# Kernel optimization log

Measured on AMD Instinct MI355X. Metric: run time of the kernel, lower is better.

The kernel has to match this reference:

```python
import jax, jax.numpy as jnp
import numpy as np

B, S, D, H, F = 8, 1024, 1024, 16, 4096
DH = D // H
LN_EPS = 1e-3  # keras LayerNormalization default


def layer_norm(x, g, b, eps=LN_EPS):
    m = jnp.mean(x, axis=-1, keepdims=True)
    v = jnp.mean(jnp.square(x - m), axis=-1, keepdims=True)
    return (x - m) * jax.lax.rsqrt(v + eps) * g + b


def setup_inputs() -> dict:
    key = jax.random.key(0)
    ks = jax.random.split(key, 16)
    s = 0.02
    return {
        "x": jax.random.normal(ks[0], (B, S, D), dtype=jnp.float32),
        "key_padding_mask": jax.random.randint(ks[1], (B, S), 0, 2) > 0,
        "wq": jax.random.normal(ks[2], (D, D), dtype=jnp.float32) * s,
        "wk": jax.random.normal(ks[3], (D, D), dtype=jnp.float32) * s,
        "wv": jax.random.normal(ks[4], (D, D), dtype=jnp.float32) * s,
        "wo": jax.random.normal(ks[5], (D, D), dtype=jnp.float32) * s,
        "gamma": jnp.ones((H,), dtype=jnp.float32),
        "ln_g": jnp.ones((3, D), dtype=jnp.float32),   # pre_attn, post_attn, pre_fc
        "ln_b": jnp.zeros((3, D), dtype=jnp.float32),
        "ln_fc_g": jnp.ones((F,), dtype=jnp.float32),  # post_fc_norm over fc_dim
        "ln_fc_b": jnp.zeros((F,), dtype=jnp.float32),
        "w1": jax.random.normal(ks[6], (D, F), dtype=jnp.float32) * s,
        "b1": jnp.zeros((F,), dtype=jnp.float32),
        "w2": jax.random.normal(ks[7], (F, D), dtype=jnp.float32) * s,
        "b2": jnp.zeros((D,), dtype=jnp.float32),
        "lam": jnp.ones((D,), dtype=jnp.float32),
    }


def reference(x, key_padding_mask, wq, wk, wv, wo, gamma, ln_g, ln_b,
              ln_fc_g, ln_fc_b, w1, b1, w2, b2, lam):
    # ---- attention sub-block (self-attention path, x_clt=None) ----
    residual = x
    h = layer_norm(x, ln_g[0], ln_b[0])                       # pre_attn_norm
    q = (h @ wq).reshape(B, S, H, DH)
    k = (h @ wk).reshape(B, S, H, DH)
    v = (h @ wv).reshape(B, S, H, DH)
    scores = jnp.einsum('bqhd,bkhd->bhqk', q, k) / jnp.sqrt(jnp.float32(DH))
    # key_padding_mask: True = masked key
    scores = jnp.where(key_padding_mask[:, None, None, :], -1e9, scores)
    v = jnp.where(key_padding_mask[:, :, None, None], 0.0, v)
    attn = jax.nn.softmax(scores, axis=-1)
    ws = jnp.einsum('bhqk,bkhd->bqhd', attn, v)
    ws = ws * gamma[None, None, :, None]                      # per-head scale
    out = ws.reshape(B, S, D) @ wo
    out = layer_norm(out, ln_g[1], ln_b[1])                   # post_attn_norm
    x = out + residual
    # ---- FFN sub-block ----
    residual = x
    h = layer_norm(x, ln_g[2], ln_b[2])                       # pre_fc_norm
    h = jax.nn.gelu(h @ w1 + b1, approximate=False)
    h = layer_norm(h, ln_fc_g, ln_fc_b)                       # post_fc_norm (fc_dim)
    h = h @ w2 + b2
    return h + residual * lam
```

## Files before the change

kernel.cpp:

```cpp
#include <hip/hip_runtime.h>
#include <math.h>

typedef _Float16 h_t;
typedef _Float16 h8 __attribute__((ext_vector_type(8)));
typedef _Float16 h4 __attribute__((ext_vector_type(4)));
typedef float    f4 __attribute__((ext_vector_type(4)));
typedef unsigned int u32;

#define SEQ   1024
#define DIM   1024
#define FDIM  4096
#define NB    8
#define NH    16
#define DHD   64
#define NROWS 8192

__device__ __forceinline__ void glds16(const void* g, void* l)
{
    __builtin_amdgcn_global_load_lds((const __attribute__((address_space(1))) u32*)g,
                                     (__attribute__((address_space(3))) u32*)l, 16, 0, 0);
}

__global__ __launch_bounds__(256)
void canon_mask_k(const void* __restrict__ raw, int* __restrict__ outm, int n)
{
    const unsigned int*  w  = (const unsigned int*)raw;
    const unsigned char* cb = (const unsigned char*)raw;
    __shared__ int flag;
    if (threadIdx.x == 0) flag = 0;
    __syncthreads();
    int bad = 0;
    for (int i = threadIdx.x; i < 1024; i += 256)
        if (w[i] > 1u) bad = 1;
    if (bad) flag = 1;
    __syncthreads();
    const bool is_i32 = (flag == 0);
    const int idx = blockIdx.x * 256 + threadIdx.x;
    if (idx < n) outm[idx] = is_i32 ? (w[idx] != 0u) : (cb[idx] != 0);
}

__global__ __launch_bounds__(256)
void wconv_k(const float* __restrict__ W, h_t* __restrict__ Wt, int K, int N)
{
    __shared__ float T[32][33];
    const int t  = threadIdx.x;
    const int k0 = blockIdx.y * 32, n0 = blockIdx.x * 32;
    const int r = t >> 3, c4 = (t & 7) * 4;
    const float4 v = *(const float4*)(W + (size_t)(k0 + r) * N + n0 + c4);
    T[r][c4 + 0] = v.x; T[r][c4 + 1] = v.y; T[r][c4 + 2] = v.z; T[r][c4 + 3] = v.w;
    __syncthreads();
    h4 o = { (h_t)T[c4 + 0][r], (h_t)T[c4 + 1][r], (h_t)T[c4 + 2][r], (h_t)T[c4 + 3][r] };
    *(h4*)(Wt + (size_t)(n0 + r) * K + k0 + c4) = o;
}

__device__ __forceinline__ void block_reduce2(float& s, float& ss)
{
    #pragma unroll
    for (int off = 32; off > 0; off >>= 1) {
        s  += __shfl_down(s,  off, 64);
        ss += __shfl_down(ss, off, 64);
    }
    __shared__ float sh[8];
    const int wid  = threadIdx.x >> 6;
    const int lane = threadIdx.x & 63;
    if (lane == 0) { sh[wid] = s; sh[4 + wid] = ss; }
    __syncthreads();
    s  = sh[0] + sh[1] + sh[2] + sh[3];
    ss = sh[4] + sh[5] + sh[6] + sh[7];
}

template<typename TI, bool RES>
__global__ __launch_bounds__(256)
void ln1024_k(const TI* __restrict__ in, const float* __restrict__ gw,
              const float* __restrict__ bw, const float* __restrict__ res,
              h_t* __restrict__ out)
{
    const size_t base = (size_t)blockIdx.x * 1024;
    const int c = threadIdx.x * 4;
    float v[4];
    if constexpr (sizeof(TI) == 2) {
        h4 x = *(const h4*)(in + base + c);
        v[0] = (float)x[0]; v[1] = (float)x[1]; v[2] = (float)x[2]; v[3] = (float)x[3];
    } else {
        float4 x = *(const float4*)((const float*)in + base + c);
        v[0] = x.x; v[1] = x.y; v[2] = x.z; v[3] = x.w;
    }
    float s = v[0] + v[1] + v[2] + v[3];
    float ss = v[0]*v[0] + v[1]*v[1] + v[2]*v[2] + v[3]*v[3];
    block_reduce2(s, ss);
    const float mean = s * (1.f / 1024.f);
    const float rstd = rsqrtf(ss * (1.f / 1024.f) - mean * mean + 1e-3f);
    const float4 g4 = *(const float4*)(gw + c);
    const float4 b4 = *(const float4*)(bw + c);
    float o[4];
    o[0] = (v[0]-mean)*rstd*g4.x + b4.x; o[1] = (v[1]-mean)*rstd*g4.y + b4.y;
    o[2] = (v[2]-mean)*rstd*g4.z + b4.z; o[3] = (v[3]-mean)*rstd*g4.w + b4.w;
    if constexpr (RES) {
        const float4 r4 = *(const float4*)(res + base + c);
        o[0] += r4.x; o[1] += r4.y; o[2] += r4.z; o[3] += r4.w;
    }
    h4 oh = {(h_t)o[0], (h_t)o[1], (h_t)o[2], (h_t)o[3]};
    *(h4*)(out + base + c) = oh;
}

__global__ __launch_bounds__(256)
void ln4096_k(h_t* __restrict__ buf, const float* __restrict__ gw,
              const float* __restrict__ bw)
{
    const size_t base = (size_t)blockIdx.x * 4096;
    const int t = threadIdx.x;
    float v[16];
    #pragma unroll
    for (int i = 0; i < 2; ++i) {
        h8 x = *(const h8*)(buf + base + (i * 256 + t) * 8);
        #pragma unroll
        for (int j = 0; j < 8; ++j) v[i * 8 + j] = (float)x[j];
    }
    float s = 0.f, ss = 0.f;
    #pragma unroll
    for (int i = 0; i < 16; ++i) { s += v[i]; ss += v[i] * v[i]; }
    block_reduce2(s, ss);
    const float mean = s * (1.f / 4096.f);
    const float rstd = rsqrtf(ss * (1.f / 4096.f) - mean * mean + 1e-3f);
    #pragma unroll
    for (int i = 0; i < 2; ++i) {
        const int c = (i * 256 + t) * 8;
        h8 o;
        #pragma unroll
        for (int j = 0; j < 8; ++j)
            o[j] = (h_t)((v[i*8+j] - mean) * rstd * gw[c + j] + bw[c + j]);
        *(h8*)(buf + base + c) = o;
    }
}

#define GEPI_QK   0
#define GEPI_VT   1
#define GEPI_H16  2
#define GEPI_GELU 3
#define GEPI_FC2  4

__device__ __forceinline__ float gelu_exact(float x)
{
    return 0.5f * x * (1.f + erff(x * 0.70710678118654752440f));
}

template<int EPI>
__global__ __launch_bounds__(256, 2)
void hgemm_k(const h_t* __restrict__ A, const h_t* __restrict__ Wt,
             const float* __restrict__ bias, void* __restrict__ outv,
             int M, int K, int N,
             const int* __restrict__ mask, const h_t* __restrict__ resid,
             const float* __restrict__ lam)
{
    __shared__ h_t As[128 * 32];
    __shared__ h_t Bs[128 * 32];
    const int t = threadIdx.x;
    const int wv = t >> 6, lane = t & 63;
    const int m0 = blockIdx.y * 128, n0 = blockIdx.x * 128;
    const int wr = (wv >> 1) * 64, wc = (wv & 1) * 64;
    const int lr = lane & 15, g = lane >> 4;
    const int srow_base = (lane >> 2);
    const int sslot = (lane & 3) * 16;

    f4 acc[4][4] = {};

    for (int k0 = 0; k0 < K; k0 += 32) {
        __syncthreads();
        #pragma unroll
        for (int i = 0; i < 2; ++i) {
            const int rA = (wv * 2 + i) * 16 + srow_base;
            const int swz = ((rA >> 1) & 3) << 4;
            glds16((const char*)A  + (((size_t)(m0 + rA) * K + k0) << 1) + (sslot ^ swz),
                   (char*)As + (wv * 2 + i) * 1024);
            glds16((const char*)Wt + (((size_t)(n0 + rA) * K + k0) << 1) + (sslot ^ swz),
                   (char*)Bs + (wv * 2 + i) * 1024);
        }
        __syncthreads();
        h8 af[4], bf[4];
        #pragma unroll
        for (int mt = 0; mt < 4; ++mt) {
            const int r = wr + mt * 16 + lr;
            af[mt] = *(const h8*)((const char*)As + r * 64 + ((g * 16) ^ (((r >> 1) & 3) << 4)));
        }
        #pragma unroll
        for (int nt = 0; nt < 4; ++nt) {
            const int r = wc + nt * 16 + lr;
            bf[nt] = *(const h8*)((const char*)Bs + r * 64 + ((g * 16) ^ (((r >> 1) & 3) << 4)));
        }
        #pragma unroll
        for (int mt = 0; mt < 4; ++mt)
            #pragma unroll
            for (int nt = 0; nt < 4; ++nt)
                acc[mt][nt] = __builtin_amdgcn_mfma_f32_16x16x32_f16(af[mt], bf[nt], acc[mt][nt], 0, 0, 0);
    }

    #pragma unroll
    for (int mt = 0; mt < 4; ++mt) {
        #pragma unroll
        for (int nt = 0; nt < 4; ++nt) {
            #pragma unroll
            for (int e = 0; e < 4; ++e) {
                const int row = m0 + wr + mt * 16 + g * 4 + e;
                const int col = n0 + wc + nt * 16 + lr;
                float val = acc[mt][nt][e];
                if constexpr (EPI == GEPI_QK) {
                    const int b = row >> 10, s = row & 1023, hh = col >> 6, dd = col & 63;
                    ((h_t*)outv)[(((size_t)(b * NH + hh)) * SEQ + s) * DHD + dd] = (h_t)val;
                } else if constexpr (EPI == GEPI_VT) {
                    if (mask[row]) val = 0.f;
                    const int b = row >> 10, s = row & 1023, hh = col >> 6, dd = col & 63;
                    ((h_t*)outv)[(((size_t)(b * NH + hh)) * DHD + dd) * SEQ + s] = (h_t)val;
                } else if constexpr (EPI == GEPI_H16) {
                    ((h_t*)outv)[(size_t)row * N + col] = (h_t)val;
                } else if constexpr (EPI == GEPI_GELU) {
                    ((h_t*)outv)[(size_t)row * N + col] = (h_t)gelu_exact(val + bias[col]);
                } else {
                    val += bias[col] + (float)resid[(size_t)row * N + col] * lam[col];
                    ((float*)outv)[(size_t)row * N + col] = val;
                }
            }
        }
    }
}

__global__ __launch_bounds__(256)
void attn_k(const h_t* __restrict__ Q, const h_t* __restrict__ K,
            const h_t* __restrict__ Vt, const int* __restrict__ mask,
            const float* __restrict__ gamma, h_t* __restrict__ out)
{
    __shared__ h_t Kt[64 * 64];
    __shared__ h_t Vs[64 * 64];
    __shared__ h_t Pl[4 * 16 * 64];
    __shared__ float madd[64];
    const int t = threadIdx.x, wv = t >> 6, lane = t & 63;
    const int lr = lane & 15, g = lane >> 4;
    const int b = blockIdx.z, h = blockIdx.y, q0 = blockIdx.x * 64;
    const size_t qkbase = ((size_t)(b * NH + h)) * SEQ * DHD;
    const size_t vbase  = ((size_t)(b * NH + h)) * DHD * SEQ;

    h8 qf[2];
    {
        const h_t* qp = Q + qkbase + (size_t)(q0 + wv * 16 + lr) * DHD;
        const h_t sc = (h_t)0.125f;
        qf[0] = *(const h8*)(qp + 8 * g) * sc;
        qf[1] = *(const h8*)(qp + 32 + 8 * g) * sc;
    }

    f4 o[4] = {};
    float mrun = -3.0e38f, lrun = 0.f;
    h_t* pw = Pl + wv * 1024;

    for (int kt = 0; kt < SEQ / 64; ++kt) {
        const int kv0 = kt * 64;
        __syncthreads();
        #pragma unroll
        for (int i = 0; i < 2; ++i) {
            const int r = (wv * 2 + i) * 8 + (lane >> 3);
            const int slot = (lane & 7) * 16;
            glds16((const char*)K  + ((qkbase + (size_t)(kv0 + r) * DHD) << 1) + (slot ^ ((r & 7) << 4)),
                   (char*)Kt + (wv * 2 + i) * 1024);
            glds16((const char*)Vt + ((vbase + (size_t)r * SEQ + kv0) << 1) + (slot ^ ((r & 7) << 4)),
                   (char*)Vs + (wv * 2 + i) * 1024);
        }
        if (t < 64) madd[t] = mask[b * SEQ + kv0 + t] ? -1e9f : 0.f;
        __syncthreads();

        f4 s[4] = {};
        #pragma unroll
        for (int tt = 0; tt < 4; ++tt) {
            #pragma unroll
            for (int c = 0; c < 2; ++c) {
                const int r = tt * 16 + lr;
                h8 kf = *(const h8*)((const char*)Kt + r * 128 + ((c * 64 + g * 16) ^ ((r & 7) << 4)));
                s[tt] = __builtin_amdgcn_mfma_f32_16x16x32_f16(kf, qf[c], s[tt], 0, 0, 0);
            }
        }
        float mt_ = -3.0e38f;
        #pragma unroll
        for (int tt = 0; tt < 4; ++tt) {
            f4 ma = *(const f4*)(&madd[tt * 16 + g * 4]);
            s[tt] += ma;
            mt_ = fmaxf(mt_, fmaxf(fmaxf(s[tt][0], s[tt][1]), fmaxf(s[tt][2], s[tt][3])));
        }
        mt_ = fmaxf(mt_, __shfl_xor(mt_, 16, 64));
        mt_ = fmaxf(mt_, __shfl_xor(mt_, 32, 64));
        const float mnew = fmaxf(mrun, mt_);
        const float scl  = __expf(mrun - mnew);
        mrun = mnew;
        float ps = 0.f;
        #pragma unroll
        for (int tt = 0; tt < 4; ++tt) {
            const float p0 = __expf(s[tt][0] - mnew), p1 = __expf(s[tt][1] - mnew);
            const float p2 = __expf(s[tt][2] - mnew), p3 = __expf(s[tt][3] - mnew);
            ps += p0 + p1 + p2 + p3;
            h4 pq = {(h_t)p0, (h_t)p1, (h_t)p2, (h_t)p3};
            *(h4*)((char*)pw + lr * 128 + ((tt * 32 + g * 8) ^ ((lr & 7) << 4))) = pq;
        }
        ps += __shfl_xor(ps, 16, 64);
        ps += __shfl_xor(ps, 32, 64);
        lrun = lrun * scl + ps;

        #pragma unroll
        for (int e = 0; e < 4; ++e) {
            const float sce = __shfl(scl, g * 4 + e, 64);
            #pragma unroll
            for (int dt = 0; dt < 4; ++dt) o[dt][e] *= sce;
        }
        #pragma unroll
        for (int c = 0; c < 2; ++c) {
            h8 pa = *(const h8*)((const char*)pw + lr * 128 + ((c * 64 + g * 16) ^ ((lr & 7) << 4)));
            #pragma unroll
            for (int dt = 0; dt < 4; ++dt) {
                const int r = dt * 16 + lr;
                h8 vf = *(const h8*)((const char*)Vs + r * 128 + ((c * 64 + g * 16) ^ ((r & 7) << 4)));
                o[dt] = __builtin_amdgcn_mfma_f32_16x16x32_f16(pa, vf, o[dt], 0, 0, 0);
            }
        }
    }
    const float gm = gamma[h];
    #pragma unroll
    for (int e = 0; e < 4; ++e) {
        const float inv = gm / __shfl(lrun, g * 4 + e, 64);
        const int row = q0 + wv * 16 + g * 4 + e;
        #pragma unroll
        for (int dt = 0; dt < 4; ++dt)
            out[(size_t)(b * SEQ + row) * DIM + h * DHD + dt * 16 + lr] = (h_t)(o[dt][e] * inv);
    }
}

extern "C" void kernel_launch(void* const* d_in, const int* in_sizes, int n_in,
                              void* d_out, int out_size, void* d_ws, size_t ws_size,
                              hipStream_t stream)
{
    const float* x       = (const float*)d_in[0];
    const void*  kpm     = d_in[1];
    const float* wq      = (const float*)d_in[2];
    const float* wk      = (const float*)d_in[3];
    const float* wv      = (const float*)d_in[4];
    const float* wo      = (const float*)d_in[5];
    const float* gamma   = (const float*)d_in[6];
    const float* ln_g    = (const float*)d_in[7];
    const float* ln_b    = (const float*)d_in[8];
    const float* ln_fc_g = (const float*)d_in[9];
    const float* ln_fc_b = (const float*)d_in[10];
    const float* w1      = (const float*)d_in[11];
    const float* b1      = (const float*)d_in[12];
    const float* w2      = (const float*)d_in[13];
    const float* b2      = (const float*)d_in[14];
    const float* lam     = (const float*)d_in[15];
    float* out = (float*)d_out;

    char* ws = (char*)d_ws;
    const size_t MB = 1 << 20;
    int* mask_i = (int*)ws;
    h_t* wqt = (h_t*)(ws + 1  * MB);
    h_t* wkt = (h_t*)(ws + 3  * MB);
    h_t* wvt = (h_t*)(ws + 5  * MB);
    h_t* wot = (h_t*)(ws + 7  * MB);
    h_t* w1t = (h_t*)(ws + 9  * MB);
    h_t* w2t = (h_t*)(ws + 17 * MB);
    h_t* bufA = (h_t*)(ws + 25 * MB);
    h_t* bufQ = (h_t*)(ws + 41 * MB);
    h_t* bufK = (h_t*)(ws + 57 * MB);
    h_t* bufV = (h_t*)(ws + 73 * MB);
    h_t* bufX2 = (h_t*)(ws + 89 * MB);

    canon_mask_k<<<NROWS / 256, 256, 0, stream>>>(kpm, mask_i, NROWS);

    wconv_k<<<dim3(32, 32),  256, 0, stream>>>(wq, wqt, DIM, DIM);
    wconv_k<<<dim3(32, 32),  256, 0, stream>>>(wk, wkt, DIM, DIM);
    wconv_k<<<dim3(32, 32),  256, 0, stream>>>(wv, wvt, DIM, DIM);
    wconv_k<<<dim3(32, 32),  256, 0, stream>>>(wo, wot, DIM, DIM);
    wconv_k<<<dim3(128, 32), 256, 0, stream>>>(w1, w1t, DIM, FDIM);
    wconv_k<<<dim3(32, 128), 256, 0, stream>>>(w2, w2t, FDIM, DIM);

    ln1024_k<float, false><<<NROWS, 256, 0, stream>>>(x, ln_g, ln_b, nullptr, bufA);

    const dim3 gqkv(DIM / 128, NROWS / 128);
    hgemm_k<GEPI_QK><<<gqkv, 256, 0, stream>>>(bufA, wqt, nullptr, bufQ, NROWS, DIM, DIM, nullptr, nullptr, nullptr);
    hgemm_k<GEPI_QK><<<gqkv, 256, 0, stream>>>(bufA, wkt, nullptr, bufK, NROWS, DIM, DIM, nullptr, nullptr, nullptr);
    hgemm_k<GEPI_VT><<<gqkv, 256, 0, stream>>>(bufA, wvt, nullptr, bufV, NROWS, DIM, DIM, mask_i, nullptr, nullptr);

    attn_k<<<dim3(SEQ / 64, NH, NB), 256, 0, stream>>>(bufQ, bufK, bufV, mask_i, gamma, bufA);

    hgemm_k<GEPI_H16><<<gqkv, 256, 0, stream>>>(bufA, wot, nullptr, bufQ, NROWS, DIM, DIM, nullptr, nullptr, nullptr);
    ln1024_k<h_t, true><<<NROWS, 256, 0, stream>>>(bufQ, ln_g + DIM, ln_b + DIM, x, bufX2);
    ln1024_k<h_t, false><<<NROWS, 256, 0, stream>>>(bufX2, ln_g + 2 * DIM, ln_b + 2 * DIM, nullptr, bufA);

    const int CH = 4096;
    for (int c = 0; c < NROWS / CH; ++c) {
        const size_t ro = (size_t)c * CH;
        hgemm_k<GEPI_GELU><<<dim3(FDIM / 128, CH / 128), 256, 0, stream>>>(
            bufA + ro * DIM, w1t, b1, bufK, CH, DIM, FDIM, nullptr, nullptr, nullptr);
        ln4096_k<<<CH, 256, 0, stream>>>(bufK, ln_fc_g, ln_fc_b);
        hgemm_k<GEPI_FC2><<<dim3(DIM / 128, CH / 128), 256, 0, stream>>>(
            bufK, w2t, b2, out + ro * DIM, CH, FDIM, DIM, nullptr, bufX2 + ro * DIM, lam);
    }
}
```

Measured before the change: 667.1 us.

## Fuse QKV GEMM and LayerNorms, deepen GEMM K-tile, remap workgroups, lazy softmax rescale

Combines the Q, K and V projections into one GEMM over a concatenated weight, with an epilogue that routes columns to the three outputs. The post-attention and pre-FC LayerNorms are merged into a single kernel. The GEMM K-tile grows from 32 to 64 with a new LDS swizzle, and workgroup IDs are remapped so tiles are grouped per XCD. The attention kernel precomputes LDS offsets, gets a 3-block occupancy hint, and skips the running-max rescale unless the max rises by more than 8. These aim to cut launches, redundant reads of the activations, loop overhead and exp/scale work, at the cost of doubled GEMM LDS (which may reduce occupancy) and a softmax that relies on the threshold for fp16 range safety.

```diff
diff --git a/kernel.cpp b/kernel.cpp
--- a/kernel.cpp
+++ b/kernel.cpp
@@ -69,22 +69,14 @@
     ss = sh[4] + sh[5] + sh[6] + sh[7];
 }
 
-template<typename TI, bool RES>
 __global__ __launch_bounds__(256)
-void ln1024_k(const TI* __restrict__ in, const float* __restrict__ gw,
-              const float* __restrict__ bw, const float* __restrict__ res,
-              h_t* __restrict__ out)
+void ln1024_k(const float* __restrict__ in, const float* __restrict__ gw,
+              const float* __restrict__ bw, h_t* __restrict__ out)
 {
     const size_t base = (size_t)blockIdx.x * 1024;
     const int c = threadIdx.x * 4;
-    float v[4];
-    if constexpr (sizeof(TI) == 2) {
-        h4 x = *(const h4*)(in + base + c);
-        v[0] = (float)x[0]; v[1] = (float)x[1]; v[2] = (float)x[2]; v[3] = (float)x[3];
-    } else {
-        float4 x = *(const float4*)((const float*)in + base + c);
-        v[0] = x.x; v[1] = x.y; v[2] = x.z; v[3] = x.w;
-    }
+    float4 xv = *(const float4*)(in + base + c);
+    float v[4] = {xv.x, xv.y, xv.z, xv.w};
     float s = v[0] + v[1] + v[2] + v[3];
     float ss = v[0]*v[0] + v[1]*v[1] + v[2]*v[2] + v[3]*v[3];
     block_reduce2(s, ss);
@@ -92,15 +84,48 @@
     const float rstd = rsqrtf(ss * (1.f / 1024.f) - mean * mean + 1e-3f);
     const float4 g4 = *(const float4*)(gw + c);
     const float4 b4 = *(const float4*)(bw + c);
-    float o[4];
-    o[0] = (v[0]-mean)*rstd*g4.x + b4.x; o[1] = (v[1]-mean)*rstd*g4.y + b4.y;
-    o[2] = (v[2]-mean)*rstd*g4.z + b4.z; o[3] = (v[3]-mean)*rstd*g4.w + b4.w;
-    if constexpr (RES) {
-        const float4 r4 = *(const float4*)(res + base + c);
-        o[0] += r4.x; o[1] += r4.y; o[2] += r4.z; o[3] += r4.w;
-    }
-    h4 oh = {(h_t)o[0], (h_t)o[1], (h_t)o[2], (h_t)o[3]};
+    h4 oh = {(h_t)((v[0]-mean)*rstd*g4.x + b4.x), (h_t)((v[1]-mean)*rstd*g4.y + b4.y),
+             (h_t)((v[2]-mean)*rstd*g4.z + b4.z), (h_t)((v[3]-mean)*rstd*g4.w + b4.w)};
     *(h4*)(out + base + c) = oh;
+}
+
+__global__ __launch_bounds__(256)
+void ln_fuse_k(const h_t* __restrict__ proj, const float* __restrict__ x,
+               const float* __restrict__ g1, const float* __restrict__ b1w,
+               const float* __restrict__ g2, const float* __restrict__ b2w,
+               h_t* __restrict__ x2out, h_t* __restrict__ h2out)
+{
+    const size_t base = (size_t)blockIdx.x * 1024;
+    const int c = threadIdx.x * 4;
+    h4 p = *(const h4*)(proj + base + c);
+    float v[4] = {(float)p[0], (float)p[1], (float)p[2], (float)p[3]};
+    float s = v[0]+v[1]+v[2]+v[3];
+    float ss = v[0]*v[0]+v[1]*v[1]+v[2]*v[2]+v[3]*v[3];
+    block_reduce2(s, ss);
+    {
+        const float mean = s * (1.f/1024.f);
+        const float rstd = rsqrtf(ss * (1.f/1024.f) - mean*mean + 1e-3f);
+        const float4 g4 = *(const float4*)(g1 + c);
+        const float4 b4 = *(const float4*)(b1w + c);
+        const float4 r4 = *(const float4*)(x + base + c);
+        v[0] = (v[0]-mean)*rstd*g4.x + b4.x + r4.x;
+        v[1] = (v[1]-mean)*rstd*g4.y + b4.y + r4.y;
+        v[2] = (v[2]-mean)*rstd*g4.z + b4.z + r4.z;
+        v[3] = (v[3]-mean)*rstd*g4.w + b4.w + r4.w;
+    }
+    h4 x2h = {(h_t)v[0], (h_t)v[1], (h_t)v[2], (h_t)v[3]};
+    *(h4*)(x2out + base + c) = x2h;
+    __syncthreads();
+    float s2 = v[0]+v[1]+v[2]+v[3];
+    float ss2 = v[0]*v[0]+v[1]*v[1]+v[2]*v[2]+v[3]*v[3];
+    block_reduce2(s2, ss2);
+    const float mean = s2 * (1.f/1024.f);
+    const float rstd = rsqrtf(ss2 * (1.f/1024.f) - mean*mean + 1e-3f);
+    const float4 g4 = *(const float4*)(g2 + c);
+    const float4 b4 = *(const float4*)(b2w + c);
+    h4 oh = {(h_t)((v[0]-mean)*rstd*g4.x + b4.x), (h_t)((v[1]-mean)*rstd*g4.y + b4.y),
+             (h_t)((v[2]-mean)*rstd*g4.z + b4.z), (h_t)((v[3]-mean)*rstd*g4.w + b4.w)};
+    *(h4*)(h2out + base + c) = oh;
 }
 
 __global__ __launch_bounds__(256)
@@ -133,8 +158,7 @@
     }
 }
 
-#define GEPI_QK   0
-#define GEPI_VT   1
+#define GEPI_QKV  0
 #define GEPI_H16  2
 #define GEPI_GELU 3
 #define GEPI_FC2  4
@@ -150,48 +174,62 @@
              const float* __restrict__ bias, void* __restrict__ outv,
              int M, int K, int N,
              const int* __restrict__ mask, const h_t* __restrict__ resid,
-             const float* __restrict__ lam)
-{
-    __shared__ h_t As[128 * 32];
-    __shared__ h_t Bs[128 * 32];
+             const float* __restrict__ lam, h_t* __restrict__ out2,
+             h_t* __restrict__ out3)
+{
+    __shared__ h_t As[128 * 64];
+    __shared__ h_t Bs[128 * 64];
     const int t = threadIdx.x;
     const int wv = t >> 6, lane = t & 63;
-    const int m0 = blockIdx.y * 128, n0 = blockIdx.x * 128;
+
+    int bx, by;
+    {
+        const int nwg = gridDim.x * gridDim.y;
+        int wg = blockIdx.y * gridDim.x + blockIdx.x;
+        const int xcd = wg & 7, rest = wg >> 3;
+        const int q = nwg >> 3, r = nwg & 7;
+        wg = (xcd < r ? xcd * (q + 1) : r * (q + 1) + (xcd - r) * q) + rest;
+        bx = wg % gridDim.x; by = wg / gridDim.x;
+    }
+    const int m0 = by * 128, n0 = bx * 128;
     const int wr = (wv >> 1) * 64, wc = (wv & 1) * 64;
     const int lr = lane & 15, g = lane >> 4;
-    const int srow_base = (lane >> 2);
-    const int sslot = (lane & 3) * 16;
+    const int sr = lane >> 3;
+    const int sslot = (lane & 7) * 16;
+    const int sswz = sr << 4;
 
     f4 acc[4][4] = {};
 
-    for (int k0 = 0; k0 < K; k0 += 32) {
+    for (int k0 = 0; k0 < K; k0 += 64) {
         __syncthreads();
         #pragma unroll
-        for (int i = 0; i < 2; ++i) {
-            const int rA = (wv * 2 + i) * 16 + srow_base;
-            const int swz = ((rA >> 1) & 3) << 4;
-            glds16((const char*)A  + (((size_t)(m0 + rA) * K + k0) << 1) + (sslot ^ swz),
-                   (char*)As + (wv * 2 + i) * 1024);
-            glds16((const char*)Wt + (((size_t)(n0 + rA) * K + k0) << 1) + (sslot ^ swz),
-                   (char*)Bs + (wv * 2 + i) * 1024);
+        for (int j = 0; j < 4; ++j) {
+            const int r = j * 32 + wv * 8 + sr;
+            glds16((const char*)A  + (((size_t)(m0 + r) * K + k0) << 1) + (sslot ^ sswz),
+                   (char*)As + j * 4096 + wv * 1024);
+            glds16((const char*)Wt + (((size_t)(n0 + r) * K + k0) << 1) + (sslot ^ sswz),
+                   (char*)Bs + j * 4096 + wv * 1024);
         }
         __syncthreads();
-        h8 af[4], bf[4];
-        #pragma unroll
-        for (int mt = 0; mt < 4; ++mt) {
-            const int r = wr + mt * 16 + lr;
-            af[mt] = *(const h8*)((const char*)As + r * 64 + ((g * 16) ^ (((r >> 1) & 3) << 4)));
-        }
-        #pragma unroll
-        for (int nt = 0; nt < 4; ++nt) {
-            const int r = wc + nt * 16 + lr;
-            bf[nt] = *(const h8*)((const char*)Bs + r * 64 + ((g * 16) ^ (((r >> 1) & 3) << 4)));
-        }
-        #pragma unroll
-        for (int mt = 0; mt < 4; ++mt)
-            #pragma unroll
-            for (int nt = 0; nt < 4; ++nt)
-                acc[mt][nt] = __builtin_amdgcn_mfma_f32_16x16x32_f16(af[mt], bf[nt], acc[mt][nt], 0, 0, 0);
+        #pragma unroll
+        for (int kk = 0; kk < 2; ++kk) {
+            h8 af[4], bf[4];
+            #pragma unroll
+            for (int mt = 0; mt < 4; ++mt) {
+                const int r = wr + mt * 16 + lr;
+                af[mt] = *(const h8*)((const char*)As + r * 128 + ((kk * 64 + g * 16) ^ ((lr & 7) << 4)));
+            }
+            #pragma unroll
+            for (int nt = 0; nt < 4; ++nt) {
+                const int r = wc + nt * 16 + lr;
+                bf[nt] = *(const h8*)((const char*)Bs + r * 128 + ((kk * 64 + g * 16) ^ ((lr & 7) << 4)));
+            }
+            #pragma unroll
+            for (int mt = 0; mt < 4; ++mt)
+                #pragma unroll
+                for (int nt = 0; nt < 4; ++nt)
+                    acc[mt][nt] = __builtin_amdgcn_mfma_f32_16x16x32_f16(af[mt], bf[nt], acc[mt][nt], 0, 0, 0);
+        }
     }
 
     #pragma unroll
@@ -203,13 +241,19 @@
                 const int row = m0 + wr + mt * 16 + g * 4 + e;
                 const int col = n0 + wc + nt * 16 + lr;
                 float val = acc[mt][nt][e];
-                if constexpr (EPI == GEPI_QK) {
-                    const int b = row >> 10, s = row & 1023, hh = col >> 6, dd = col & 63;
-                    ((h_t*)outv)[(((size_t)(b * NH + hh)) * SEQ + s) * DHD + dd] = (h_t)val;
-                } else if constexpr (EPI == GEPI_VT) {
-                    if (mask[row]) val = 0.f;
-                    const int b = row >> 10, s = row & 1023, hh = col >> 6, dd = col & 63;
-                    ((h_t*)outv)[(((size_t)(b * NH + hh)) * DHD + dd) * SEQ + s] = (h_t)val;
+                if constexpr (EPI == GEPI_QKV) {
+                    const int matm = col >> 10;
+                    const int cc = col & 1023;
+                    const int b = row >> 10, s = row & 1023;
+                    const int hh = cc >> 6, dd = cc & 63;
+                    if (matm == 0)
+                        ((h_t*)outv)[(((size_t)(b * NH + hh)) * SEQ + s) * DHD + dd] = (h_t)val;
+                    else if (matm == 1)
+                        out2[(((size_t)(b * NH + hh)) * SEQ + s) * DHD + dd] = (h_t)val;
+                    else {
+                        if (mask[row]) val = 0.f;
+                        out3[(((size_t)(b * NH + hh)) * DHD + dd) * SEQ + s] = (h_t)val;
+                    }
                 } else if constexpr (EPI == GEPI_H16) {
                     ((h_t*)outv)[(size_t)row * N + col] = (h_t)val;
                 } else if constexpr (EPI == GEPI_GELU) {
@@ -223,7 +267,7 @@
     }
 }
 
-__global__ __launch_bounds__(256)
+__global__ __launch_bounds__(256, 3)
 void attn_k(const h_t* __restrict__ Q, const h_t* __restrict__ K,
             const h_t* __restrict__ Vt, const int* __restrict__ mask,
             const float* __restrict__ gamma, h_t* __restrict__ out)
@@ -246,6 +290,23 @@
         qf[1] = *(const h8*)(qp + 32 + 8 * g) * sc;
     }
 
+    int koff[4][2], poff[4], paoff[2];
+    #pragma unroll
+    for (int tt = 0; tt < 4; ++tt) {
+        const int r = tt * 16 + lr;
+        const int sw = (r & 7) << 4;
+        koff[tt][0] = r * 128 + ((g * 16) ^ sw);
+        koff[tt][1] = r * 128 + ((64 + g * 16) ^ sw);
+        poff[tt] = lr * 128 + (((tt * 32 + g * 8)) ^ ((lr & 7) << 4));
+    }
+    #pragma unroll
+    for (int c = 0; c < 2; ++c)
+        paoff[c] = lr * 128 + ((c * 64 + g * 16) ^ ((lr & 7) << 4));
+
+    const int sgr = lane >> 3;
+    const int sgslot = (lane & 7) * 16;
+    const int sgswz = sgr << 4;
+
     f4 o[4] = {};
     float mrun = -3.0e38f, lrun = 0.f;
     h_t* pw = Pl + wv * 1024;
@@ -255,11 +316,10 @@
         __syncthreads();
         #pragma unroll
         for (int i = 0; i < 2; ++i) {
-            const int r = (wv * 2 + i) * 8 + (lane >> 3);
-            const int slot = (lane & 7) * 16;
-            glds16((const char*)K  + ((qkbase + (size_t)(kv0 + r) * DHD) << 1) + (slot ^ ((r & 7) << 4)),
+            const int r = (wv * 2 + i) * 8 + sgr;
+            glds16((const char*)K  + ((qkbase + (size_t)(kv0 + r) * DHD) << 1) + (sgslot ^ sgswz),
                    (char*)Kt + (wv * 2 + i) * 1024);
-            glds16((const char*)Vt + ((vbase + (size_t)r * SEQ + kv0) << 1) + (slot ^ ((r & 7) << 4)),
+            glds16((const char*)Vt + ((vbase + (size_t)r * SEQ + kv0) << 1) + (sgslot ^ sgswz),
                    (char*)Vs + (wv * 2 + i) * 1024);
         }
         if (t < 64) madd[t] = mask[b * SEQ + kv0 + t] ? -1e9f : 0.f;
@@ -267,14 +327,12 @@
 
         f4 s[4] = {};
         #pragma unroll
-        for (int tt = 0; tt < 4; ++tt) {
+        for (int tt = 0; tt < 4; ++tt)
             #pragma unroll
             for (int c = 0; c < 2; ++c) {
-                const int r = tt * 16 + lr;
-                h8 kf = *(const h8*)((const char*)Kt + r * 128 + ((c * 64 + g * 16) ^ ((r & 7) << 4)));
+                h8 kf = *(const h8*)((const char*)Kt + koff[tt][c]);
                 s[tt] = __builtin_amdgcn_mfma_f32_16x16x32_f16(kf, qf[c], s[tt], 0, 0, 0);
             }
-        }
         float mt_ = -3.0e38f;
         #pragma unroll
         for (int tt = 0; tt < 4; ++tt) {
@@ -284,35 +342,42 @@
         }
         mt_ = fmaxf(mt_, __shfl_xor(mt_, 16, 64));
         mt_ = fmaxf(mt_, __shfl_xor(mt_, 32, 64));
-        const float mnew = fmaxf(mrun, mt_);
-        const float scl  = __expf(mrun - mnew);
-        mrun = mnew;
+
+        const bool skip = __all(mt_ <= mrun + 8.f);
+        float scl = 1.f;
+        if (!skip) {
+            const float mnew = fmaxf(mrun, mt_);
+            scl = __expf(mrun - mnew);
+            mrun = mnew;
+        }
         float ps = 0.f;
         #pragma unroll
         for (int tt = 0; tt < 4; ++tt) {
-            const float p0 = __expf(s[tt][0] - mnew), p1 = __expf(s[tt][1] - mnew);
-            const float p2 = __expf(s[tt][2] - mnew), p3 = __expf(s[tt][3] - mnew);
+            const float p0 = __expf(s[tt][0] - mrun), p1 = __expf(s[tt][1] - mrun);
+            const float p2 = __expf(s[tt][2] - mrun), p3 = __expf(s[tt][3] - mrun);
             ps += p0 + p1 + p2 + p3;
             h4 pq = {(h_t)p0, (h_t)p1, (h_t)p2, (h_t)p3};
-            *(h4*)((char*)pw + lr * 128 + ((tt * 32 + g * 8) ^ ((lr & 7) << 4))) = pq;
+            *(h4*)((char*)pw + poff[tt]) = pq;
         }
         ps += __shfl_xor(ps, 16, 64);
         ps += __shfl_xor(ps, 32, 64);
-        lrun = lrun * scl + ps;
-
-        #pragma unroll
-        for (int e = 0; e < 4; ++e) {
-            const float sce = __shfl(scl, g * 4 + e, 64);
-            #pragma unroll
-            for (int dt = 0; dt < 4; ++dt) o[dt][e] *= sce;
+        if (skip) {
+            lrun += ps;
+        } else {
+            lrun = lrun * scl + ps;
+            #pragma unroll
+            for (int e = 0; e < 4; ++e) {
+                const float sce = __shfl(scl, g * 4 + e, 64);
+                #pragma unroll
+                for (int dt = 0; dt < 4; ++dt) o[dt][e] *= sce;
+            }
         }
         #pragma unroll
         for (int c = 0; c < 2; ++c) {
-            h8 pa = *(const h8*)((const char*)pw + lr * 128 + ((c * 64 + g * 16) ^ ((lr & 7) << 4)));
+            h8 pa = *(const h8*)((const char*)pw + paoff[c]);
             #pragma unroll
             for (int dt = 0; dt < 4; ++dt) {
-                const int r = dt * 16 + lr;
-                h8 vf = *(const h8*)((const char*)Vs + r * 128 + ((c * 64 + g * 16) ^ ((r & 7) << 4)));
+                h8 vf = *(const h8*)((const char*)Vs + koff[dt][c]);
                 o[dt] = __builtin_amdgcn_mfma_f32_16x16x32_f16(pa, vf, o[dt], 0, 0, 0);
             }
         }
@@ -353,9 +418,10 @@
     char* ws = (char*)d_ws;
     const size_t MB = 1 << 20;
     int* mask_i = (int*)ws;
-    h_t* wqt = (h_t*)(ws + 1  * MB);
-    h_t* wkt = (h_t*)(ws + 3  * MB);
-    h_t* wvt = (h_t*)(ws + 5  * MB);
+    h_t* wqkvt = (h_t*)(ws + 1  * MB);
+    h_t* wqt = wqkvt;
+    h_t* wkt = wqkvt + (size_t)1024 * 1024;
+    h_t* wvt = wqkvt + (size_t)2048 * 1024;
     h_t* wot = (h_t*)(ws + 7  * MB);
     h_t* w1t = (h_t*)(ws + 9  * MB);
     h_t* w2t = (h_t*)(ws + 17 * MB);
@@ -374,26 +440,26 @@
     wconv_k<<<dim3(128, 32), 256, 0, stream>>>(w1, w1t, DIM, FDIM);
     wconv_k<<<dim3(32, 128), 256, 0, stream>>>(w2, w2t, FDIM, DIM);
 
-    ln1024_k<float, false><<<NROWS, 256, 0, stream>>>(x, ln_g, ln_b, nullptr, bufA);
-
-    const dim3 gqkv(DIM / 128, NROWS / 128);
-    hgemm_k<GEPI_QK><<<gqkv, 256, 0, stream>>>(bufA, wqt, nullptr, bufQ, NROWS, DIM, DIM, nullptr, nullptr, nullptr);
-    hgemm_k<GEPI_QK><<<gqkv, 256, 0, stream>>>(bufA, wkt, nullptr, bufK, NROWS, DIM, DIM, nullptr, nullptr, nullptr);
-    hgemm_k<GEPI_VT><<<gqkv, 256, 0, stream>>>(bufA, wvt, nullptr, bufV, NROWS, DIM, DIM, mask_i, nullptr, nullptr);
+    ln1024_k<<<NROWS, 256, 0, stream>>>(x, ln_g, ln_b, bufA);
+
+    hgemm_k<GEPI_QKV><<<dim3(3072 / 128, NROWS / 128), 256, 0, stream>>>(
+        bufA, wqkvt, nullptr, bufQ, NROWS, DIM, 3072, mask_i, nullptr, nullptr, bufK, bufV);
 
     attn_k<<<dim3(SEQ / 64, NH, NB), 256, 0, stream>>>(bufQ, bufK, bufV, mask_i, gamma, bufA);
 
-    hgemm_k<GEPI_H16><<<gqkv, 256, 0, stream>>>(bufA, wot, nullptr, bufQ, NROWS, DIM, DIM, nullptr, nullptr, nullptr);
-    ln1024_k<h_t, true><<<NROWS, 256, 0, stream>>>(bufQ, ln_g + DIM, ln_b + DIM, x, bufX2);
-    ln1024_k<h_t, false><<<NROWS, 256, 0, stream>>>(bufX2, ln_g + 2 * DIM, ln_b + 2 * DIM, nullptr, bufA);
+    hgemm_k<GEPI_H16><<<dim3(DIM / 128, NROWS / 128), 256, 0, stream>>>(
+        bufA, wot, nullptr, bufQ, NROWS, DIM, DIM, nullptr, nullptr, nullptr, nullptr, nullptr);
+
+    ln_fuse_k<<<NROWS, 256, 0, stream>>>(bufQ, x, ln_g + DIM, ln_b + DIM,
+                                         ln_g + 2 * DIM, ln_b + 2 * DIM, bufX2, bufA);
 
     const int CH = 4096;
     for (int c = 0; c < NROWS / CH; ++c) {
         const size_t ro = (size_t)c * CH;
         hgemm_k<GEPI_GELU><<<dim3(FDIM / 128, CH / 128), 256, 0, stream>>>(
-            bufA + ro * DIM, w1t, b1, bufK, CH, DIM, FDIM, nullptr, nullptr, nullptr);
+            bufA + ro * DIM, w1t, b1, bufK, CH, DIM, FDIM, nullptr, nullptr, nullptr, nullptr, nullptr);
         ln4096_k<<<CH, 256, 0, stream>>>(bufK, ln_fc_g, ln_fc_b);
         hgemm_k<GEPI_FC2><<<dim3(DIM / 128, CH / 128), 256, 0, stream>>>(
-            bufK, w2t, b2, out + ro * DIM, CH, FDIM, DIM, nullptr, bufX2 + ro * DIM, lam);
-    }
-}
+            bufK, w2t, b2, out + ro * DIM, CH, FDIM, DIM, nullptr, bufX2 + ro * DIM, lam, nullptr, nullptr);
+    }
+}
```

Result: faster. 637.6 us (-4.4%).
